# Kernel tuning notes

Measured on AMD Instinct MI355X. Metric: run time of the kernel, lower is better.

The kernel has to match this reference:

```python
import jax, jax.numpy as jnp
import numpy as np

DIM = 1024
N_HEADS = 16
HEAD_DIM = DIM // N_HEADS
LN_EPS = 1e-5


def layer_norm(x, gamma, beta):
    mu = jnp.mean(x, axis=-1, keepdims=True)
    var = jnp.var(x, axis=-1, keepdims=True)
    return (x - mu) * jax.lax.rsqrt(var + LN_EPS) * gamma + beta


def setup_inputs() -> dict:
    key = jax.random.key(0)
    ks = jax.random.split(key, 12)
    B, Nq, Nc, D = 2, 2048, 2048, DIM
    s = 1.0 / np.sqrt(D)
    return {
        "query": jax.random.normal(ks[0], (B, Nq, D), jnp.float32),
        "context": jax.random.normal(ks[1], (B, Nc, D), jnp.float32),
        "Wq": jax.random.normal(ks[2], (D, D), jnp.float32) * s,
        "bq": jnp.zeros((D,), jnp.float32),
        "Wk": jax.random.normal(ks[3], (D, D), jnp.float32) * s,
        "bk": jnp.zeros((D,), jnp.float32),
        "Wv": jax.random.normal(ks[4], (D, D), jnp.float32) * s,
        "bv": jnp.zeros((D,), jnp.float32),
        "Wo": jax.random.normal(ks[5], (D, D), jnp.float32) * s,
        "bo": jnp.zeros((D,), jnp.float32),
        "gq": jnp.ones((D,), jnp.float32),
        "betaq": jnp.zeros((D,), jnp.float32),
        "gkv": jnp.ones((D,), jnp.float32),
        "betakv": jnp.zeros((D,), jnp.float32),
    }


def reference(query, context, Wq, bq, Wk, bk, Wv, bv, Wo, bo, gq, betaq, gkv, betakv):
    B, Nq, D = query.shape
    Nc = context.shape[1]
    residual = query
    q = layer_norm(query, gq, betaq)
    c = layer_norm(context, gkv, betakv)
    # projections; (B,N,D) -> (B,H,N,hd)
    Q = (q @ Wq + bq).reshape(B, Nq, N_HEADS, HEAD_DIM).transpose(0, 2, 1, 3)
    K = (c @ Wk + bk).reshape(B, Nc, N_HEADS, HEAD_DIM).transpose(0, 2, 1, 3)
    V = (c @ Wv + bv).reshape(B, Nc, N_HEADS, HEAD_DIM).transpose(0, 2, 1, 3)
    scores = jnp.einsum("bhqd,bhkd->bhqk", Q, K) / np.sqrt(HEAD_DIM).astype(np.float32)
    attn = jax.nn.softmax(scores, axis=-1)
    out = jnp.einsum("bhqk,bhkd->bhqd", attn, V)
    out = out.transpose(0, 2, 1, 3).reshape(B, Nq, D)
    return residual + out @ Wo + bo
```

## Files before the change

kernel.cpp:

```cpp
#include <hip/hip_runtime.h>
#include <hip/hip_bf16.h>

typedef unsigned short u16;
typedef unsigned long long u64;
typedef __bf16 bf16x8 __attribute__((ext_vector_type(8)));
typedef float f32x4 __attribute__((ext_vector_type(4)));

#define DIM 1024
#define NH 16
#define HD 64
#define QSCALE 0.180336880972788f

__device__ __forceinline__ u16 f2bf(float f) {
  union { float f; unsigned u; } v; v.f = f;
  unsigned r = v.u + 0x7fffu + ((v.u >> 16) & 1u);
  return (u16)(r >> 16);
}

__device__ __forceinline__ unsigned pk2(float a, float b) {
  union { __hip_bfloat162 h; unsigned u; } cv;
  cv.h = __float22bfloat162_rn(make_float2(a, b));
  return cv.u;
}

__device__ __forceinline__ void gld16(const u16* gp, u16* lp) {
  __builtin_amdgcn_global_load_lds(
      (const __attribute__((address_space(1))) unsigned int*)(const void*)gp,
      (__attribute__((address_space(3))) unsigned int*)(void*)lp, 16, 0, 0);
}

__global__ __launch_bounds__(256) void prep_kernel(
    const float* __restrict__ q, const float* __restrict__ c,
    const float* __restrict__ gq, const float* __restrict__ bq,
    const float* __restrict__ gkv, const float* __restrict__ bkv,
    u16* __restrict__ qn, u16* __restrict__ cn,
    const float* W0, const float* W1, const float* W2, const float* W3,
    u16* O0, u16* O1, u16* O2, u16* O3) {
  __shared__ float red[2][4];
  __shared__ float t[32][33];
  int bid = blockIdx.x, tid = threadIdx.x;
  if (bid < 8192) {
    const float* x  = bid < 4096 ? q : c;
    const float* g  = bid < 4096 ? gq : gkv;
    const float* be = bid < 4096 ? bq : bkv;
    u16* out = bid < 4096 ? qn : cn;
    int row = bid & 4095;
    float4 v = ((const float4*)(x + (size_t)row * DIM))[tid];
    float s1 = v.x + v.y + v.z + v.w;
    float s2 = v.x * v.x + v.y * v.y + v.z * v.z + v.w * v.w;
#pragma unroll
    for (int o = 32; o >= 1; o >>= 1) { s1 += __shfl_xor(s1, o, 64); s2 += __shfl_xor(s2, o, 64); }
    int wv = tid >> 6;
    if ((tid & 63) == 0) { red[0][wv] = s1; red[1][wv] = s2; }
    __syncthreads();
    s1 = red[0][0] + red[0][1] + red[0][2] + red[0][3];
    s2 = red[1][0] + red[1][1] + red[1][2] + red[1][3];
    float mu = s1 * (1.f / DIM);
    float var = s2 * (1.f / DIM) - mu * mu;
    float rs = rsqrtf(var + 1e-5f);
    float4 gv = ((const float4*)g)[tid];
    float4 bv = ((const float4*)be)[tid];
    uint2 o2;
    o2.x = pk2((v.x - mu) * rs * gv.x + bv.x, (v.y - mu) * rs * gv.y + bv.y);
    o2.y = pk2((v.z - mu) * rs * gv.z + bv.z, (v.w - mu) * rs * gv.w + bv.w);
    ((uint2*)(out + (size_t)row * DIM))[tid] = o2;
  } else {
    int wid = bid - 8192;
    int z = wid >> 10;
    const float* W = z == 0 ? W0 : z == 1 ? W1 : z == 2 ? W2 : W3;
    u16* O        = z == 0 ? O0 : z == 1 ? O1 : z == 2 ? O2 : O3;
    int xy = wid & 1023;
    int bx = (xy & 31) * 32, by = (xy >> 5) * 32;
    int tx = tid & 31, ty = tid >> 5;
#pragma unroll
    for (int i = 0; i < 4; ++i) t[ty + i * 8][tx] = W[(size_t)(by + ty + i * 8) * DIM + bx + tx];
    __syncthreads();
#pragma unroll
    for (int i = 0; i < 4; ++i) O[(size_t)(bx + ty + i * 8) * DIM + by + tx] = f2bf(t[tx][ty + i * 8]);
  }
}

struct GArg { const u16* A; const u16* Bt; const float* bias; void* out; const float* resid; int mode; };
struct GArg3 { GArg g[3]; };

__global__ __launch_bounds__(256) void gemm128(GArg3 args) {
  GArg ga = args.g[blockIdx.z];
  const u16* __restrict__ A  = ga.A;
  const u16* __restrict__ Bt = ga.Bt;
  __shared__ __align__(16) u16 sm[(128 + 64) * 64];
  u16* As = sm;
  u16* Bs = sm + 128 * 64;
  int tid = threadIdx.x, wave = tid >> 6, lane = tid & 63;
  int lr = lane & 15, quad = lane >> 4;
  int m0 = blockIdx.x * 128, n0 = blockIdx.y * 64;
  int wm = (wave >> 1) * 64, wn = (wave & 1) * 32;
  f32x4 acc[4][2] = {};
  for (int kt = 0; kt < DIM; kt += 64) {
#pragma unroll
    for (int r = 0; r < 4; ++r) {
      int slot = tid + r * 256;
      int row = slot >> 3;
      int c = (slot & 7) ^ (row & 7);
      gld16(A + (size_t)(m0 + row) * DIM + kt + c * 8, &As[slot * 8]);
    }
#pragma unroll
    for (int r = 0; r < 2; ++r) {
      int slot = tid + r * 256;
      int row = slot >> 3;
      int c = (slot & 7) ^ (row & 7);
      gld16(Bt + (size_t)(n0 + row) * DIM + kt + c * 8, &Bs[slot * 8]);
    }
    __syncthreads();
#pragma unroll
    for (int kc = 0; kc < 2; ++kc) {
      int pc = ((kc * 4 + quad) ^ (lr & 7)) * 8;
      bf16x8 af[4], bfr[2];
#pragma unroll
      for (int i = 0; i < 4; ++i) af[i] = *(const bf16x8*)&As[(wm + i * 16 + lr) * 64 + pc];
#pragma unroll
      for (int j = 0; j < 2; ++j) bfr[j] = *(const bf16x8*)&Bs[(wn + j * 16 + lr) * 64 + pc];
#pragma unroll
      for (int mi = 0; mi < 4; ++mi)
#pragma unroll
        for (int ni = 0; ni < 2; ++ni)
          acc[mi][ni] = __builtin_amdgcn_mfma_f32_16x16x32_bf16(af[mi], bfr[ni], acc[mi][ni], 0, 0, 0);
    }
    __syncthreads();
  }
  int mode = ga.mode;
  const float* bias = ga.bias;
#pragma unroll
  for (int mi = 0; mi < 4; ++mi)
#pragma unroll
    for (int ni = 0; ni < 2; ++ni) {
      int col = n0 + wn + ni * 16 + lr;
      float bv = bias[col];
      int row0 = m0 + wm + mi * 16 + quad * 4;
      if (mode == 2) {
        int bb = row0 >> 11, t0 = row0 & 2047;
        u64 pk = 0;
#pragma unroll
        for (int r = 0; r < 4; ++r)
          pk |= (u64)f2bf(acc[mi][ni][r] + bv) << (16 * r);
        *(u64*)&((u16*)ga.out)[((size_t)(bb << 10) + col) * 2048 + t0] = pk;
      } else if (mode == 3) {
#pragma unroll
        for (int r = 0; r < 4; ++r) {
          int row = row0 + r;
          ((float*)ga.out)[(size_t)row * DIM + col] =
              acc[mi][ni][r] + bv + ga.resid[(size_t)row * DIM + col];
        }
      } else {
        float sc = (mode == 1) ? QSCALE : 1.f;
#pragma unroll
        for (int r = 0; r < 4; ++r)
          ((u16*)ga.out)[(size_t)(row0 + r) * DIM + col] = f2bf((acc[mi][ni][r] + bv) * sc);
      }
    }
}

#define FK0 0
#define FV0 4096
#define FK1 8192
#define FV1 12288
#define FQP 16384
__global__ __launch_bounds__(256) void flash_kernel(const u16* __restrict__ Q,
    const u16* __restrict__ Kg, const u16* __restrict__ Vt, u16* __restrict__ AO) {
  __shared__ __align__(16) u16 lds[24576];
  int tid = threadIdx.x, wave = tid >> 6, lane = tid & 63;
  int lr = lane & 15, quad = lane >> 4;
  int bh = blockIdx.x, b = bh >> 4, h = bh & 15;
  int q0 = blockIdx.y * 128;

  const u16* qbase = Q + (size_t)(b * 2048 + q0) * DIM + h * HD;
  const u16* kbase = Kg + (size_t)(b * 2048) * DIM + h * HD;
  const u16* vbase = Vt + (size_t)(b * 1024 + h * HD) * 2048;

#pragma unroll
  for (int r = 0; r < 4; ++r) {
    int slot = tid + r * 256;
    int row = slot >> 3;
    int c = (slot & 7) ^ (row & 7);
    gld16(qbase + (size_t)row * DIM + c * 8, &lds[FQP + slot * 8]);
  }
#pragma unroll
  for (int r = 0; r < 2; ++r) {
    int slot = tid + r * 256;
    int row = slot >> 3;
    int c = (slot & 7) ^ (row & 7);
    gld16(kbase + (size_t)row * DIM + c * 8, &lds[FK0 + slot * 8]);
    gld16(vbase + (size_t)row * 2048 + c * 8, &lds[FV0 + slot * 8]);
  }
  __syncthreads();

  bf16x8 qf[2][2];
#pragma unroll
  for (int s = 0; s < 2; ++s)
#pragma unroll
    for (int kc = 0; kc < 2; ++kc)
      qf[s][kc] = *(const bf16x8*)&lds[FQP + (wave * 32 + s * 16 + lr) * 64 +
                                       (((kc * 4 + quad) ^ (lr & 7)) * 8)];

  int pb = FQP + wave * 2048;
  float plsum[2] = {0.f, 0.f};
  f32x4 oacc[2][4] = {};

  for (int j = 0; j < 32; ++j) {
    int cb = (j & 1) ? FK1 : FK0;
    if (j < 31) {
      int nb = (j & 1) ? FK0 : FK1;
      int nj = j * 64 + 64;
#pragma unroll
      for (int r = 0; r < 2; ++r) {
        int slot = tid + r * 256;
        int row = slot >> 3;
        int c = (slot & 7) ^ (row & 7);
        gld16(kbase + (size_t)(nj + row) * DIM + c * 8, &lds[nb + slot * 8]);
        gld16(vbase + (size_t)row * 2048 + nj + c * 8, &lds[nb + 4096 + slot * 8]);
      }
    }

    f32x4 sf[2][4] = {};
#pragma unroll
    for (int kc = 0; kc < 2; ++kc) {
      int pc = ((kc * 4 + quad) ^ (lr & 7)) * 8;
#pragma unroll
      for (int ns = 0; ns < 4; ++ns) {
        bf16x8 kf = *(const bf16x8*)&lds[cb + (ns * 16 + lr) * 64 + pc];
#pragma unroll
        for (int s = 0; s < 2; ++s)
          sf[s][ns] = __builtin_amdgcn_mfma_f32_16x16x32_bf16(kf, qf[s][kc], sf[s][ns], 0, 0, 0);
      }
    }

#pragma unroll
    for (int s = 0; s < 2; ++s)
#pragma unroll
      for (int ns = 0; ns < 4; ++ns) {
        float p0 = exp2f(sf[s][ns][0]), p1 = exp2f(sf[s][ns][1]);
        float p2 = exp2f(sf[s][ns][2]), p3 = exp2f(sf[s][ns][3]);
        plsum[s] += (p0 + p1) + (p2 + p3);
        uint2 pk;
        pk.x = pk2(p0, p1);
        pk.y = pk2(p2, p3);
        int chunk = ns * 2 + (quad >> 1);
        int off = pb + (s * 16 + lr) * 64 + ((chunk ^ (lr & 7)) * 8) + (quad & 1) * 4;
        *(uint2*)&lds[off] = pk;
      }
    __threadfence_block();

#pragma unroll
    for (int kc = 0; kc < 2; ++kc) {
      int pc = ((kc * 4 + quad) ^ (lr & 7)) * 8;
      bf16x8 pf[2];
#pragma unroll
      for (int s = 0; s < 2; ++s)
        pf[s] = *(const bf16x8*)&lds[pb + (s * 16 + lr) * 64 + pc];
#pragma unroll
      for (int ds = 0; ds < 4; ++ds) {
        bf16x8 vf = *(const bf16x8*)&lds[cb + 4096 + (ds * 16 + lr) * 64 + pc];
#pragma unroll
        for (int s = 0; s < 2; ++s)
          oacc[s][ds] = __builtin_amdgcn_mfma_f32_16x16x32_bf16(vf, pf[s], oacc[s][ds], 0, 0, 0);
      }
    }
    __syncthreads();
  }

#pragma unroll
  for (int s = 0; s < 2; ++s) {
    float l = plsum[s];
    l += __shfl_xor(l, 16, 64);
    l += __shfl_xor(l, 32, 64);
    float rl = 1.f / l;
    size_t qrow = (size_t)(b * 2048 + q0 + wave * 32 + s * 16 + lr);
#pragma unroll
    for (int ds = 0; ds < 4; ++ds) {
      uint2 pk;
      pk.x = pk2(oacc[s][ds][0] * rl, oacc[s][ds][1] * rl);
      pk.y = pk2(oacc[s][ds][2] * rl, oacc[s][ds][3] * rl);
      *(uint2*)&AO[qrow * DIM + h * HD + ds * 16 + quad * 4] = pk;
    }
  }
}

extern "C" void kernel_launch(void* const* d_in, const int* in_sizes, int n_in,
                              void* d_out, int out_size, void* d_ws, size_t ws_size,
                              hipStream_t stream) {
  const float* query   = (const float*)d_in[0];
  const float* context = (const float*)d_in[1];
  const float* Wq = (const float*)d_in[2];
  const float* bq = (const float*)d_in[3];
  const float* Wk = (const float*)d_in[4];
  const float* bk = (const float*)d_in[5];
  const float* Wv = (const float*)d_in[6];
  const float* bv = (const float*)d_in[7];
  const float* Wo = (const float*)d_in[8];
  const float* bo = (const float*)d_in[9];
  const float* gq    = (const float*)d_in[10];
  const float* betaq = (const float*)d_in[11];
  const float* gkv   = (const float*)d_in[12];
  const float* betakv= (const float*)d_in[13];
  (void)in_sizes; (void)n_in; (void)out_size; (void)ws_size;

  char* ws = (char*)d_ws;
  const size_t MB = (size_t)1 << 20;
  u16* qn  = (u16*)(ws + 0 * MB);
  u16* cn  = (u16*)(ws + 8 * MB);
  u16* Wqt = (u16*)(ws + 16 * MB);
  u16* Wkt = (u16*)(ws + 18 * MB);
  u16* Wvt = (u16*)(ws + 20 * MB);
  u16* Wot = (u16*)(ws + 22 * MB);
  u16* Qb  = (u16*)(ws + 24 * MB);
  u16* Kb  = (u16*)(ws + 32 * MB);
  u16* Vtb = (u16*)(ws + 40 * MB);
  u16* AOb = (u16*)(ws + 48 * MB);

  prep_kernel<<<12288, 256, 0, stream>>>(query, context, gq, betaq, gkv, betakv,
                                         qn, cn, Wq, Wk, Wv, Wo, Wqt, Wkt, Wvt, Wot);

  GArg3 a3;
  a3.g[0] = { qn, Wqt, bq, (void*)Qb,  nullptr, 1 };
  a3.g[1] = { cn, Wkt, bk, (void*)Kb,  nullptr, 0 };
  a3.g[2] = { cn, Wvt, bv, (void*)Vtb, nullptr, 2 };
  gemm128<<<dim3(32, 16, 3), 256, 0, stream>>>(a3);

  flash_kernel<<<dim3(32, 16), 256, 0, stream>>>(Qb, Kb, Vtb, AOb);

  GArg3 ao;
  ao.g[0] = { AOb, Wot, bo, d_out, query, 3 };
  ao.g[1] = ao.g[0];
  ao.g[2] = ao.g[0];
  gemm128<<<dim3(32, 16, 1), 256, 0, stream>>>(ao);
}
```

Measured before the change: 248.9 us.

## Split flash attention over two KV halves with combine kernel, widen QKV GEMM tiles

```diff
diff --git a/kernel.cpp b/kernel.cpp
--- a/kernel.cpp
+++ b/kernel.cpp
@@ -21,6 +21,10 @@
   union { __hip_bfloat162 h; unsigned u; } cv;
   cv.h = __float22bfloat162_rn(make_float2(a, b));
   return cv.u;
+}
+
+__device__ __forceinline__ float bf2f(unsigned s) {
+  union { unsigned u; float f; } v; v.u = s << 16; return v.f;
 }
 
 __device__ __forceinline__ void gld16(const u16* gp, u16* lp) {
@@ -80,13 +84,82 @@
   }
 }
 
-struct GArg { const u16* A; const u16* Bt; const float* bias; void* out; const float* resid; int mode; };
+struct GArg { const u16* A; const u16* Bt; const float* bias; void* out; int mode; };
 struct GArg3 { GArg g[3]; };
 
 __global__ __launch_bounds__(256) void gemm128(GArg3 args) {
   GArg ga = args.g[blockIdx.z];
   const u16* __restrict__ A  = ga.A;
   const u16* __restrict__ Bt = ga.Bt;
+  __shared__ __align__(16) u16 sm[128 * 64 * 2];
+  u16* As = sm;
+  u16* Bs = sm + 128 * 64;
+  int tid = threadIdx.x, wave = tid >> 6, lane = tid & 63;
+  int lr = lane & 15, quad = lane >> 4;
+  int m0 = blockIdx.x * 128, n0 = blockIdx.y * 128;
+  int wm = (wave >> 1) * 64, wn = (wave & 1) * 64;
+  f32x4 acc[4][4] = {};
+  for (int kt = 0; kt < DIM; kt += 64) {
+#pragma unroll
+    for (int r = 0; r < 4; ++r) {
+      int slot = tid + r * 256;
+      int row = slot >> 3;
+      int c = (slot & 7) ^ (row & 7);
+      gld16(A + (size_t)(m0 + row) * DIM + kt + c * 8, &As[slot * 8]);
+    }
+#pragma unroll
+    for (int r = 0; r < 4; ++r) {
+      int slot = tid + r * 256;
+      int row = slot >> 3;
+      int c = (slot & 7) ^ (row & 7);
+      gld16(Bt + (size_t)(n0 + row) * DIM + kt + c * 8, &Bs[slot * 8]);
+    }
+    __syncthreads();
+#pragma unroll
+    for (int kc = 0; kc < 2; ++kc) {
+      int pc = ((kc * 4 + quad) ^ (lr & 7)) * 8;
+      bf16x8 af[4], bfr[4];
+#pragma unroll
+      for (int i = 0; i < 4; ++i) {
+        af[i]  = *(const bf16x8*)&As[(wm + i * 16 + lr) * 64 + pc];
+        bfr[i] = *(const bf16x8*)&Bs[(wn + i * 16 + lr) * 64 + pc];
+      }
+#pragma unroll
+      for (int mi = 0; mi < 4; ++mi)
+#pragma unroll
+        for (int ni = 0; ni < 4; ++ni)
+          acc[mi][ni] = __builtin_amdgcn_mfma_f32_16x16x32_bf16(af[mi], bfr[ni], acc[mi][ni], 0, 0, 0);
+    }
+    __syncthreads();
+  }
+  int mode = ga.mode;
+  const float* bias = ga.bias;
+#pragma unroll
+  for (int mi = 0; mi < 4; ++mi)
+#pragma unroll
+    for (int ni = 0; ni < 4; ++ni) {
+      int col = n0 + wn + ni * 16 + lr;
+      float bv = bias[col];
+      int row0 = m0 + wm + mi * 16 + quad * 4;
+      if (mode == 2) {
+        int bb = row0 >> 11, t0 = row0 & 2047;
+        u64 pk = 0;
+#pragma unroll
+        for (int r = 0; r < 4; ++r)
+          pk |= (u64)f2bf(acc[mi][ni][r] + bv) << (16 * r);
+        *(u64*)&((u16*)ga.out)[((size_t)(bb << 10) + col) * 2048 + t0] = pk;
+      } else {
+        float sc = (mode == 1) ? QSCALE : 1.f;
+#pragma unroll
+        for (int r = 0; r < 4; ++r)
+          ((u16*)ga.out)[(size_t)(row0 + r) * DIM + col] = f2bf((acc[mi][ni][r] + bv) * sc);
+      }
+    }
+}
+
+__global__ __launch_bounds__(256) void gemm_o(const u16* __restrict__ A,
+    const u16* __restrict__ Bt, const float* __restrict__ bias,
+    float* __restrict__ out, const float* __restrict__ resid) {
   __shared__ __align__(16) u16 sm[(128 + 64) * 64];
   u16* As = sm;
   u16* Bs = sm + 128 * 64;
@@ -127,8 +200,6 @@
     }
     __syncthreads();
   }
-  int mode = ga.mode;
-  const float* bias = ga.bias;
 #pragma unroll
   for (int mi = 0; mi < 4; ++mi)
 #pragma unroll
@@ -136,25 +207,10 @@
       int col = n0 + wn + ni * 16 + lr;
       float bv = bias[col];
       int row0 = m0 + wm + mi * 16 + quad * 4;
-      if (mode == 2) {
-        int bb = row0 >> 11, t0 = row0 & 2047;
-        u64 pk = 0;
-#pragma unroll
-        for (int r = 0; r < 4; ++r)
-          pk |= (u64)f2bf(acc[mi][ni][r] + bv) << (16 * r);
-        *(u64*)&((u16*)ga.out)[((size_t)(bb << 10) + col) * 2048 + t0] = pk;
-      } else if (mode == 3) {
-#pragma unroll
-        for (int r = 0; r < 4; ++r) {
-          int row = row0 + r;
-          ((float*)ga.out)[(size_t)row * DIM + col] =
-              acc[mi][ni][r] + bv + ga.resid[(size_t)row * DIM + col];
-        }
-      } else {
-        float sc = (mode == 1) ? QSCALE : 1.f;
-#pragma unroll
-        for (int r = 0; r < 4; ++r)
-          ((u16*)ga.out)[(size_t)(row0 + r) * DIM + col] = f2bf((acc[mi][ni][r] + bv) * sc);
+#pragma unroll
+      for (int r = 0; r < 4; ++r) {
+        int row = row0 + r;
+        out[(size_t)row * DIM + col] = acc[mi][ni][r] + bv + resid[(size_t)row * DIM + col];
       }
     }
 }
@@ -165,16 +221,22 @@
 #define FV1 12288
 #define FQP 16384
 __global__ __launch_bounds__(256) void flash_kernel(const u16* __restrict__ Q,
-    const u16* __restrict__ Kg, const u16* __restrict__ Vt, u16* __restrict__ AO) {
+    const u16* __restrict__ Kg, const u16* __restrict__ Vt,
+    u16* __restrict__ O0, u16* __restrict__ O1,
+    float* __restrict__ L0, float* __restrict__ L1) {
   __shared__ __align__(16) u16 lds[24576];
   int tid = threadIdx.x, wave = tid >> 6, lane = tid & 63;
   int lr = lane & 15, quad = lane >> 4;
   int bh = blockIdx.x, b = bh >> 4, h = bh & 15;
   int q0 = blockIdx.y * 128;
+  int split = blockIdx.z;
+  u16* Op = split ? O1 : O0;
+  float* Lp = split ? L1 : L0;
+  int t0 = split * 1024;
 
   const u16* qbase = Q + (size_t)(b * 2048 + q0) * DIM + h * HD;
-  const u16* kbase = Kg + (size_t)(b * 2048) * DIM + h * HD;
-  const u16* vbase = Vt + (size_t)(b * 1024 + h * HD) * 2048;
+  const u16* kbase = Kg + (size_t)(b * 2048 + t0) * DIM + h * HD;
+  const u16* vbase = Vt + (size_t)(b * 1024 + h * HD) * 2048 + t0;
 
 #pragma unroll
   for (int r = 0; r < 4; ++r) {
@@ -205,9 +267,9 @@
   float plsum[2] = {0.f, 0.f};
   f32x4 oacc[2][4] = {};
 
-  for (int j = 0; j < 32; ++j) {
+  for (int j = 0; j < 16; ++j) {
     int cb = (j & 1) ? FK1 : FK0;
-    if (j < 31) {
+    if (j < 15) {
       int nb = (j & 1) ? FK0 : FK1;
       int nj = j * 64 + 64;
 #pragma unroll
@@ -272,16 +334,34 @@
     float l = plsum[s];
     l += __shfl_xor(l, 16, 64);
     l += __shfl_xor(l, 32, 64);
-    float rl = 1.f / l;
     size_t qrow = (size_t)(b * 2048 + q0 + wave * 32 + s * 16 + lr);
+    if (quad == 0) Lp[qrow * 16 + h] = l;
 #pragma unroll
     for (int ds = 0; ds < 4; ++ds) {
       uint2 pk;
-      pk.x = pk2(oacc[s][ds][0] * rl, oacc[s][ds][1] * rl);
-      pk.y = pk2(oacc[s][ds][2] * rl, oacc[s][ds][3] * rl);
-      *(uint2*)&AO[qrow * DIM + h * HD + ds * 16 + quad * 4] = pk;
-    }
-  }
+      pk.x = pk2(oacc[s][ds][0], oacc[s][ds][1]);
+      pk.y = pk2(oacc[s][ds][2], oacc[s][ds][3]);
+      *(uint2*)&Op[qrow * DIM + h * HD + ds * 16 + quad * 4] = pk;
+    }
+  }
+}
+
+__global__ __launch_bounds__(256) void combine_kernel(const u16* __restrict__ O0,
+    const u16* __restrict__ O1, const float* __restrict__ L0, const float* __restrict__ L1,
+    u16* __restrict__ AO) {
+  int row = blockIdx.x, tid = threadIdx.x;
+  int h = tid >> 4;
+  float rl = 1.f / (L0[row * 16 + h] + L1[row * 16 + h]);
+  uint2 a = ((const uint2*)(O0 + (size_t)row * DIM))[tid];
+  uint2 b = ((const uint2*)(O1 + (size_t)row * DIM))[tid];
+  float v0 = (bf2f(a.x & 0xffff) + bf2f(b.x & 0xffff)) * rl;
+  float v1 = (bf2f(a.x >> 16)    + bf2f(b.x >> 16))    * rl;
+  float v2 = (bf2f(a.y & 0xffff) + bf2f(b.y & 0xffff)) * rl;
+  float v3 = (bf2f(a.y >> 16)    + bf2f(b.y >> 16))    * rl;
+  uint2 o;
+  o.x = pk2(v0, v1);
+  o.y = pk2(v2, v3);
+  ((uint2*)(AO + (size_t)row * DIM))[tid] = o;
 }
 
 extern "C" void kernel_launch(void* const* d_in, const int* in_sizes, int n_in,
@@ -315,21 +395,23 @@
   u16* Kb  = (u16*)(ws + 32 * MB);
   u16* Vtb = (u16*)(ws + 40 * MB);
   u16* AOb = (u16*)(ws + 48 * MB);
+  u16* Op0 = qn;
+  u16* Op1 = cn;
+  float* L0 = (float*)(ws + 16 * MB);
+  float* L1 = (float*)(ws + 16 * MB + 256 * 1024);
 
   prep_kernel<<<12288, 256, 0, stream>>>(query, context, gq, betaq, gkv, betakv,
                                          qn, cn, Wq, Wk, Wv, Wo, Wqt, Wkt, Wvt, Wot);
 
   GArg3 a3;
-  a3.g[0] = { qn, Wqt, bq, (void*)Qb,  nullptr, 1 };
-  a3.g[1] = { cn, Wkt, bk, (void*)Kb,  nullptr, 0 };
-  a3.g[2] = { cn, Wvt, bv, (void*)Vtb, nullptr, 2 };
-  gemm128<<<dim3(32, 16, 3), 256, 0, stream>>>(a3);
-
-  flash_kernel<<<dim3(32, 16), 256, 0, stream>>>(Qb, Kb, Vtb, AOb);
-
-  GArg3 ao;
-  ao.g[0] = { AOb, Wot, bo, d_out, query, 3 };
-  ao.g[1] = ao.g[0];
-  ao.g[2] = ao.g[0];
-  gemm128<<<dim3(32, 16, 1), 256, 0, stream>>>(ao);
-}
+  a3.g[0] = { qn, Wqt, bq, (void*)Qb,  1 };
+  a3.g[1] = { cn, Wkt, bk, (void*)Kb,  0 };
+  a3.g[2] = { cn, Wvt, bv, (void*)Vtb, 2 };
+  gemm128<<<dim3(32, 8, 3), 256, 0, stream>>>(a3);
+
+  flash_kernel<<<dim3(32, 16, 2), 256, 0, stream>>>(Qb, Kb, Vtb, Op0, Op1, L0, L1);
+
+  combine_kernel<<<4096, 256, 0, stream>>>(Op0, Op1, L0, L1, AOb);
+
+  gemm_o<<<dim3(32, 16), 256, 0, stream>>>(AOb, Wot, bo, (float*)d_out, query);
+}
```

New measurement: 244.9 us. About the same (-1.6%).
